# Kernel optimization log

Measured on AMD Instinct MI355X. Metric: run time of the kernel, lower is better.

The kernel has to match this reference:

```python
import jax, jax.numpy as jnp
import numpy as np

NUM_HEADS = 16


def setup_inputs() -> dict:
    key = jax.random.key(0)
    k1, k2, k3 = jax.random.split(key, 3)
    T, B, E = 2048, 2, 1024
    x = jax.random.normal(k1, (T, B, E), dtype=jnp.float32)
    in_proj_w = jax.random.normal(k2, (E, 3 * E), dtype=jnp.float32) * (E ** -0.5)
    in_proj_b = jnp.zeros((3 * E,), dtype=jnp.float32)
    out_w = jax.random.normal(k3, (E, E), dtype=jnp.float32) * (E ** -0.5)
    out_b = jnp.zeros((E,), dtype=jnp.float32)
    return {"x": x, "in_proj_w": in_proj_w, "in_proj_b": in_proj_b,
            "out_w": out_w, "out_b": out_b}


def reference(x, in_proj_w, in_proj_b, out_w, out_b):
    # x: (tgt_len, bsz, embed_dim) -- seq-first, self-attention (q is k is v)
    T, B, E = x.shape
    H = NUM_HEADS
    D = E // H
    scaling = D ** -0.5
    # packed in-projection: einsum('bne,ef->bnf') over (T,B,E)
    proj = jnp.einsum('tbe,ef->tbf', x, in_proj_w) + in_proj_b
    q, k, v = jnp.split(proj, 3, axis=-1)  # each (T, B, E)
    # reshape to (T, B*H, D) then transpose to (B*H, T, D)
    q = q.reshape(T, B * H, D).transpose(1, 0, 2)
    k = k.reshape(T, B * H, D).transpose(1, 0, 2)
    v = v.reshape(T, B * H, D).transpose(1, 0, 2)
    # full O(T^2) attention matrix, scaling applied after QK^T as in source
    attn = jnp.einsum('bie,bje->bij', q, k) * scaling  # (B*H, T, T)
    attn = jax.nn.softmax(attn, axis=-1)
    out = jnp.einsum('bij,bje->bie', attn, v)  # (B*H, T, D)
    # faithful to source: reshape directly (no head transpose-back)
    out = out.reshape(B, T, E)
    out = jnp.einsum('bte,ef->btf', out, out_w) + out_b
    return out
```

## Files before the change

### kernel.cpp

```cpp
#include <hip/hip_runtime.h>
#include <stdint.h>

#define TSEQ 2048
#define NB 2
#define EMB 1024
#define NHEAD 16
#define HDIM 64
#define KSPLIT 4
#define NT (TSEQ / KSPLIT / 64)
#define QSCALE 0.18033688f

typedef __bf16 bf16x8 __attribute__((ext_vector_type(8)));
typedef __bf16 bf16x4 __attribute__((ext_vector_type(4)));
typedef float f32x4 __attribute__((ext_vector_type(4)));
typedef float f32x16 __attribute__((ext_vector_type(16)));
typedef unsigned int u32x4 __attribute__((ext_vector_type(4)));

__device__ __forceinline__ void gload_lds16(const void* g, void* lds) {
    __builtin_amdgcn_global_load_lds(
        (const __attribute__((address_space(1))) unsigned int*)g,
        (__attribute__((address_space(3))) unsigned int*)lds, 16, 0, 0);
}

__device__ __forceinline__ float fast_exp2(float x) {
#if __has_builtin(__builtin_amdgcn_exp2f)
    return __builtin_amdgcn_exp2f(x);
#else
    return exp2f(x);
#endif
}

__device__ __forceinline__ unsigned cvt_pk_bf16(float lo, float hi) {
    unsigned r;
    asm("v_cvt_pk_bf16_f32 %0, %1, %2" : "=v"(r) : "v"(lo), "v"(hi));
    return r;
}

__device__ __forceinline__ void swap32(unsigned& a, unsigned& b) {
    asm("v_permlane32_swap_b32 %0, %1" : "+v"(a), "+v"(b));
}

__device__ __forceinline__ bf16x8 as_bf16x8(u32x4 u) {
    union { u32x4 u; bf16x8 h; } c;
    c.u = u;
    return c.h;
}

__global__ __launch_bounds__(256) void prep_kernel(
    const float* __restrict__ x, const float* __restrict__ w_in,
    const float* __restrict__ w_out,
    __bf16* __restrict__ xb, __bf16* __restrict__ wiT, __bf16* __restrict__ whT)
{
    __shared__ float tile[32][33];
    int bid = blockIdx.x;
    const int tid = threadIdx.x;
    if (bid < 4096) {
        const size_t idx = ((size_t)bid * 256 + tid) * 4;
        float4 v = *(const float4*)(x + idx);
        bf16x4 o = { (__bf16)v.x, (__bf16)v.y, (__bf16)v.z, (__bf16)v.w };
        *(bf16x4*)(xb + idx) = o;
        return;
    }
    bid -= 4096;
    int bx = bid & 127;
    const int by = bid >> 7;
    const float* src; __bf16* dst; int sn;
    if (bx < 96) { src = w_in;  dst = wiT; sn = 3072; }
    else         { bx -= 96; src = w_out; dst = whT; sn = 1024; }
    const int tx = tid & 31, ty = tid >> 5;
    #pragma unroll
    for (int i = 0; i < 4; ++i)
        tile[ty + i * 8][tx] = src[(size_t)(by * 32 + ty + i * 8) * sn + bx * 32 + tx];
    __syncthreads();
    #pragma unroll
    for (int i = 0; i < 4; ++i) {
        float v = tile[tx][ty + i * 8];
        dst[(size_t)(bx * 32 + ty + i * 8) * 1024 + by * 32 + tx] = (__bf16)v;
    }
}

__global__ __launch_bounds__(256) void gemm_qkv_kernel(
    const __bf16* __restrict__ A, const __bf16* __restrict__ BT,
    const float* __restrict__ bias,
    __bf16* __restrict__ Oq, __bf16* __restrict__ Ok, __bf16* __restrict__ Ov)
{
    __shared__ __align__(16) __bf16 As[128 * 64];
    __shared__ __align__(16) __bf16 Bs[128 * 64];
    const int tid = threadIdx.x;
    const int wave = tid >> 6, lane = tid & 63;
    const int l16 = lane & 15, quad = lane >> 4;
    const int wm = wave >> 1, wn = wave & 1;
    const int m0 = blockIdx.y * 128, n0 = blockIdx.x * 128;

    f32x4 acc[4][4];
    #pragma unroll
    for (int mt = 0; mt < 4; ++mt)
        #pragma unroll
        for (int nt = 0; nt < 4; ++nt)
            #pragma unroll
            for (int r = 0; r < 4; ++r) acc[mt][nt][r] = 0.f;

    int smrow[4], schunk[4], sbase[4];
    #pragma unroll
    for (int i = 0; i < 4; ++i) {
        int linear = (wave * 4 + i) * 64 + lane;
        smrow[i] = linear >> 3;
        schunk[i] = (linear & 7) ^ (smrow[i] & 7);
        sbase[i] = (wave * 4 + i) * 512;
    }

    for (int k0 = 0; k0 < 1024; k0 += 64) {
        #pragma unroll
        for (int i = 0; i < 4; ++i) {
            gload_lds16(A + (size_t)(m0 + smrow[i]) * 1024 + k0 + schunk[i] * 8,
                        As + sbase[i]);
            gload_lds16(BT + (size_t)(n0 + smrow[i]) * 1024 + k0 + schunk[i] * 8,
                        Bs + sbase[i]);
        }
        __syncthreads();
        #pragma unroll
        for (int kk = 0; kk < 2; ++kk) {
            bf16x8 am[4], bn[4];
            #pragma unroll
            for (int mt = 0; mt < 4; ++mt) {
                int row = wm * 64 + mt * 16 + l16;
                int c = (kk * 4 + quad) ^ (row & 7);
                am[mt] = *(const bf16x8*)(As + row * 64 + c * 8);
            }
            #pragma unroll
            for (int nt = 0; nt < 4; ++nt) {
                int row = wn * 64 + nt * 16 + l16;
                int c = (kk * 4 + quad) ^ (row & 7);
                bn[nt] = *(const bf16x8*)(Bs + row * 64 + c * 8);
            }
            #pragma unroll
            for (int mt = 0; mt < 4; ++mt)
                #pragma unroll
                for (int nt = 0; nt < 4; ++nt)
                    acc[mt][nt] = __builtin_amdgcn_mfma_f32_16x16x32_bf16(
                        am[mt], bn[nt], acc[mt][nt], 0, 0, 0);
        }
        __syncthreads();
    }

    #pragma unroll
    for (int nt = 0; nt < 4; ++nt) {
        const int col = n0 + wn * 64 + nt * 16 + l16;
        const float bv = bias[col];
        const int sec = col >> 10, f = col & 1023;
        const int h = f >> 6, d = f & 63;
        #pragma unroll
        for (int mt = 0; mt < 4; ++mt)
            #pragma unroll
            for (int r = 0; r < 4; ++r) {
                const int row = m0 + wm * 64 + mt * 16 + quad * 4 + r;
                float v = acc[mt][nt][r] + bv;
                const int t = row >> 1, b = row & 1;
                const int bh = b * NHEAD + h;
                const size_t idx = ((size_t)bh * TSEQ + t) * HDIM + d;
                if (sec == 0)
                    Oq[idx] = (__bf16)(v * QSCALE);
                else if (sec == 1)
                    Ok[idx] = (__bf16)v;
                else
                    Ov[idx] = (__bf16)v;
            }
    }
}

__global__ __launch_bounds__(256) void vtrans_kernel(
    const __bf16* __restrict__ V, __bf16* __restrict__ Vt)
{
    __shared__ __bf16 T[64 * 67];
    const int bh = blockIdx.y;
    const int t0 = blockIdx.x * 64;
    const int tid = threadIdx.x;
    const int r = tid >> 2;
    const int c = (tid & 3) * 16;
    const __bf16* src = V + ((size_t)bh * TSEQ + t0 + r) * HDIM + c;
    bf16x8 a = *(const bf16x8*)src;
    bf16x8 b = *(const bf16x8*)(src + 8);
    #pragma unroll
    for (int j = 0; j < 8; ++j) {
        T[r * 67 + c + j] = a[j];
        T[r * 67 + c + 8 + j] = b[j];
    }
    __syncthreads();
    const int dr = tid >> 2;
    const int tc = (tid & 3) * 16;
    bf16x8 o0, o1;
    #pragma unroll
    for (int j = 0; j < 8; ++j) {
        o0[j] = T[(tc + j) * 67 + dr];
        o1[j] = T[(tc + 8 + j) * 67 + dr];
    }
    __bf16* dst = Vt + ((size_t)bh * HDIM + dr) * TSEQ + t0 + tc;
    *(bf16x8*)dst = o0;
    *(bf16x8*)(dst + 8) = o1;
}

__global__ __launch_bounds__(256, 2) void attn_mfma_kernel(
    const __bf16* __restrict__ Q, const __bf16* __restrict__ K,
    const __bf16* __restrict__ Vt,
    __bf16* __restrict__ O0, __bf16* __restrict__ O1,
    __bf16* __restrict__ O2, __bf16* __restrict__ O3,
    float* __restrict__ L0, float* __restrict__ L1,
    float* __restrict__ L2, float* __restrict__ L3)
{
    __shared__ __align__(16) __bf16 Ks[2][64 * 64];
    __shared__ __align__(16) __bf16 Vs[2][64 * 64];

    const int tid  = threadIdx.x;
    const int wave = tid >> 6;
    const int lane = tid & 63;
    const int l31  = lane & 31;
    const int hi   = lane >> 5;
    const int m7   = l31 & 7;

    const int lid = blockIdx.x;
    const int xcd = lid & 7;
    const int j   = lid >> 3;
    const int grp = xcd * 16 + (j >> 3);
    const int qb  = j & 7;
    const int bh  = grp >> 2;
    const int z   = grp & 3;

    const int q0   = qb * 256 + wave * 64;
    const int kbase0 = z * (TSEQ / KSPLIT);

    __bf16* __restrict__ Opart = (z == 0) ? O0 : (z == 1) ? O1 : (z == 2) ? O2 : O3;
    float*  __restrict__ Lpart = (z == 0) ? L0 : (z == 1) ? L1 : (z == 2) ? L2 : L3;

    bf16x8 qf[2][4];
    #pragma unroll
    for (int g = 0; g < 2; ++g) {
        const __bf16* Qrow =
            Q + ((size_t)bh * TSEQ + q0 + g * 32 + l31) * HDIM + 8 * hi;
        #pragma unroll
        for (int c = 0; c < 4; ++c)
            qf[g][c] = *(const bf16x8*)(Qrow + 16 * c);
    }

    f32x16 Oacc[2][2];
    #pragma unroll
    for (int g = 0; g < 2; ++g)
        #pragma unroll
        for (int dt = 0; dt < 2; ++dt)
            #pragma unroll
            for (int r = 0; r < 16; ++r) Oacc[g][dt][r] = 0.f;
    float l4[2][4] = {{0.f, 0.f, 0.f, 0.f}, {0.f, 0.f, 0.f, 0.f}};

    const __bf16* Kbase = K + ((size_t)bh * TSEQ + kbase0) * HDIM;
    const __bf16* Vbase = Vt + (size_t)bh * HDIM * TSEQ + kbase0;

    int srow[2], schk[2];
    #pragma unroll
    for (int i = 0; i < 2; ++i) {
        const int s = wave * 2 + i;
        srow[i] = s * 8 + (lane >> 3);
        schk[i] = (lane & 7) ^ (srow[i] & 7);
    }

#define STAGE(buf, kt)                                                        \
    {                                                                         \
        _Pragma("unroll")                                                     \
        for (int i = 0; i < 2; ++i) {                                         \
            const int s = wave * 2 + i;                                       \
            gload_lds16(Kbase + (size_t)((kt) * 64 + srow[i]) * HDIM          \
                            + schk[i] * 8,                                    \
                        &Ks[buf][s * 512]);                                   \
            gload_lds16(Vbase + (size_t)srow[i] * TSEQ + (kt) * 64            \
                            + schk[i] * 8,                                    \
                        &Vs[buf][s * 512]);                                   \
        }                                                                     \
    }

#define SOFTMAX(sa, g, s)                                                     \
    {                                                                         \
        float p[16];                                                          \
        _Pragma("unroll")                                                     \
        for (int r = 0; r < 16; ++r) {                                        \
            p[r] = fast_exp2((sa)[r]);                                        \
            l4[g][r & 3] += p[r];                                             \
        }                                                                     \
        unsigned x[8];                                                        \
        _Pragma("unroll")                                                     \
        for (int i = 0; i < 8; ++i)                                           \
            x[i] = cvt_pk_bf16(p[2 * i], p[2 * i + 1]);                       \
        swap32(x[0], x[2]); swap32(x[1], x[3]);                               \
        swap32(x[4], x[6]); swap32(x[5], x[7]);                               \
        pa[g][2 * (s)][0] = x[0]; pa[g][2 * (s)][1] = x[1];                   \
        pa[g][2 * (s)][2] = x[2]; pa[g][2 * (s)][3] = x[3];                   \
        pa[g][2 * (s) + 1][0] = x[4]; pa[g][2 * (s) + 1][1] = x[5];           \
        pa[g][2 * (s) + 1][2] = x[6]; pa[g][2 * (s) + 1][3] = x[7];           \
    }

    STAGE(0, 0);

    for (int kt = 0; kt < NT; ++kt) {
        const int b = kt & 1;
        __syncthreads();
        if (kt + 1 < NT) STAGE(b ^ 1, kt + 1);

        u32x4 pa[2][4];
        #pragma unroll
        for (int s = 0; s < 2; ++s) {
            f32x16 sa0, sa1;
            #pragma unroll
            for (int r = 0; r < 16; ++r) { sa0[r] = 0.f; sa1[r] = 0.f; }
            #pragma unroll
            for (int c = 0; c < 4; ++c) {
                bf16x8 kf = *(const bf16x8*)(
                    &Ks[b][(32 * s + l31) * 64 + (((c << 1) | hi) ^ m7) * 8]);
                sa0 = __builtin_amdgcn_mfma_f32_32x32x16_bf16(
                    kf, qf[0][c], sa0, 0, 0, 0);
                sa1 = __builtin_amdgcn_mfma_f32_32x32x16_bf16(
                    kf, qf[1][c], sa1, 0, 0, 0);
            }
            SOFTMAX(sa0, 0, s);
            SOFTMAX(sa1, 1, s);
        }

        #pragma unroll
        for (int dt = 0; dt < 2; ++dt)
            #pragma unroll
            for (int ks = 0; ks < 4; ++ks) {
                bf16x8 vf = *(const bf16x8*)(
                    &Vs[b][(dt * 32 + l31) * 64 + (((ks << 1) | hi) ^ m7) * 8]);
                Oacc[0][dt] = __builtin_amdgcn_mfma_f32_32x32x16_bf16(
                    as_bf16x8(pa[0][ks]), vf, Oacc[0][dt], 0, 0, 0);
                Oacc[1][dt] = __builtin_amdgcn_mfma_f32_32x32x16_bf16(
                    as_bf16x8(pa[1][ks]), vf, Oacc[1][dt], 0, 0, 0);
            }
    }
#undef STAGE
#undef SOFTMAX

    #pragma unroll
    for (int g = 0; g < 2; ++g) {
        float v = (l4[g][0] + l4[g][1]) + (l4[g][2] + l4[g][3]);
        v += __shfl_xor(v, 32);
        if (hi == 0)
            Lpart[(size_t)bh * TSEQ + q0 + g * 32 + l31] = v;
    }

    const size_t base = ((size_t)bh * TSEQ + q0) * HDIM;
    #pragma unroll
    for (int g = 0; g < 2; ++g)
        #pragma unroll
        for (int dt = 0; dt < 2; ++dt)
            #pragma unroll
            for (int r = 0; r < 16; ++r) {
                const int q = g * 32 + (r & 3) + 8 * (r >> 2) + 4 * hi;
                Opart[base + (size_t)q * HDIM + dt * 32 + l31] =
                    (__bf16)Oacc[g][dt][r];
            }
}

__global__ __launch_bounds__(256) void normalize_kernel(
    const __bf16* __restrict__ O0, const __bf16* __restrict__ O1,
    const __bf16* __restrict__ O2, const __bf16* __restrict__ O3,
    const float* __restrict__ L0, const float* __restrict__ L1,
    const float* __restrict__ L2, const float* __restrict__ L3,
    __bf16* __restrict__ Ob)
{
    const size_t gid = (size_t)blockIdx.x * 256 + threadIdx.x;
    const size_t idx = gid * 8;
    const size_t qi = idx >> 6;
    const float inv = 1.f / (L0[qi] + L1[qi] + L2[qi] + L3[qi]);
    bf16x8 a = *(const bf16x8*)(O0 + idx);
    bf16x8 b = *(const bf16x8*)(O1 + idx);
    bf16x8 c = *(const bf16x8*)(O2 + idx);
    bf16x8 d = *(const bf16x8*)(O3 + idx);
    bf16x8 o;
    #pragma unroll
    for (int j = 0; j < 8; ++j)
        o[j] = (__bf16)((((float)a[j] + (float)b[j]) +
                         ((float)c[j] + (float)d[j])) * inv);
    *(bf16x8*)(Ob + idx) = o;
}

__global__ __launch_bounds__(256) void gemm_out_kernel(
    const __bf16* __restrict__ A, const __bf16* __restrict__ BT,
    const float* __restrict__ bias, float* __restrict__ out)
{
    __shared__ __align__(16) __bf16 As[128 * 64];
    __shared__ __align__(16) __bf16 Bs[128 * 64];
    const int tid = threadIdx.x;
    const int wave = tid >> 6, lane = tid & 63;
    const int l16 = lane & 15, quad = lane >> 4;
    const int wm = wave >> 1, wn = wave & 1;
    const int m0 = blockIdx.y * 128, n0 = blockIdx.x * 128;

    f32x4 acc[4][4];
    #pragma unroll
    for (int mt = 0; mt < 4; ++mt)
        #pragma unroll
        for (int nt = 0; nt < 4; ++nt)
            #pragma unroll
            for (int r = 0; r < 4; ++r) acc[mt][nt][r] = 0.f;

    int smrow[4], schunk[4], sbase[4];
    #pragma unroll
    for (int i = 0; i < 4; ++i) {
        int linear = (wave * 4 + i) * 64 + lane;
        smrow[i] = linear >> 3;
        schunk[i] = (linear & 7) ^ (smrow[i] & 7);
        sbase[i] = (wave * 4 + i) * 512;
    }

    for (int k0 = 0; k0 < 1024; k0 += 64) {
        #pragma unroll
        for (int i = 0; i < 4; ++i) {
            gload_lds16(A + (size_t)(m0 + smrow[i]) * 1024 + k0 + schunk[i] * 8,
                        As + sbase[i]);
            gload_lds16(BT + (size_t)(n0 + smrow[i]) * 1024 + k0 + schunk[i] * 8,
                        Bs + sbase[i]);
        }
        __syncthreads();
        #pragma unroll
        for (int kk = 0; kk < 2; ++kk) {
            bf16x8 am[4], bn[4];
            #pragma unroll
            for (int mt = 0; mt < 4; ++mt) {
                int row = wm * 64 + mt * 16 + l16;
                int c = (kk * 4 + quad) ^ (row & 7);
                am[mt] = *(const bf16x8*)(As + row * 64 + c * 8);
            }
            #pragma unroll
            for (int nt = 0; nt < 4; ++nt) {
                int row = wn * 64 + nt * 16 + l16;
                int c = (kk * 4 + quad) ^ (row & 7);
                bn[nt] = *(const bf16x8*)(Bs + row * 64 + c * 8);
            }
            #pragma unroll
            for (int mt = 0; mt < 4; ++mt)
                #pragma unroll
                for (int nt = 0; nt < 4; ++nt)
                    acc[mt][nt] = __builtin_amdgcn_mfma_f32_16x16x32_bf16(
                        am[mt], bn[nt], acc[mt][nt], 0, 0, 0);
        }
        __syncthreads();
    }

    #pragma unroll
    for (int nt = 0; nt < 4; ++nt) {
        const int col = n0 + wn * 64 + nt * 16 + l16;
        const float bv = bias[col];
        #pragma unroll
        for (int mt = 0; mt < 4; ++mt)
            #pragma unroll
            for (int r = 0; r < 4; ++r) {
                const int row = m0 + wm * 64 + mt * 16 + quad * 4 + r;
                out[(size_t)row * 1024 + col] = acc[mt][nt][r] + bv;
            }
    }
}

extern "C" void kernel_launch(void* const* d_in, const int* in_sizes, int n_in,
                              void* d_out, int out_size, void* d_ws, size_t ws_size,
                              hipStream_t stream) {
    const float* x     = (const float*)d_in[0];
    const float* w_in  = (const float*)d_in[1];
    const float* b_in  = (const float*)d_in[2];
    const float* w_out = (const float*)d_in[3];
    const float* b_out = (const float*)d_in[4];
    float* out = (float*)d_out;

    const size_t M1 = (size_t)1024 * 1024;
    __bf16* ws  = (__bf16*)d_ws;
    __bf16* xb  = ws;
    __bf16* wiT = xb  + 4 * M1;
    __bf16* whT = wiT + 3 * M1;
    __bf16* Qb  = whT + 1 * M1;
    __bf16* Kb  = Qb  + 4 * M1;
    __bf16* Vt  = Kb  + 4 * M1;
    __bf16* O0  = Vt  + 4 * M1;
    __bf16* O1  = O0  + 4 * M1;
    float*  L0  = (float*)(O1 + 4 * M1);
    float*  L1  = L0 + 65536;
    float*  L2  = L1 + 65536;
    float*  L3  = L2 + 65536;
    __bf16* Vb  = (__bf16*)d_out;
    __bf16* O2  = (__bf16*)d_out;
    __bf16* O3  = O2 + 4 * M1;
    __bf16* Ob  = xb;

    prep_kernel<<<8192, 256, 0, stream>>>(x, w_in, w_out, xb, wiT, whT);
    gemm_qkv_kernel<<<dim3(24, 32), 256, 0, stream>>>(
        xb, wiT, b_in, Qb, Kb, Vb);
    vtrans_kernel<<<dim3(32, 32), 256, 0, stream>>>(Vb, Vt);
    attn_mfma_kernel<<<dim3(1024), 256, 0, stream>>>(
        Qb, Kb, Vt, O0, O1, O2, O3, L0, L1, L2, L3);
    normalize_kernel<<<2048, 256, 0, stream>>>(
        O0, O1, O2, O3, L0, L1, L2, L3, Ob);
    gemm_out_kernel<<<dim3(8, 32), 256, 0, stream>>>(
        Ob, whT, b_out, out);
}
```

Baseline: 200.9 us.

## Use 512-thread attention blocks with triple-buffered K/V staging and MFMA priority

The attention kernel now runs 8 waves per block covering 512 query rows, so each staged K/V tile is shared by twice as many waves and each wave issues one load per tile. K/V staging moves from double to triple buffering with a two-tile prefetch distance, using an explicit vmcnt wait plus s_barrier in place of __syncthreads. s_setprio is raised around the MFMA sections so they are favoured over softmax work from other waves. In exchange LDS per block grows, the launch bound asks for 4 blocks of 512 threads per CU, which tightens the register budget, and the hand-written waitcnt depends on the exact number of outstanding loads.

Result: slower. 427.5 us (+112.8%).

```diff
diff --git a/kernel.cpp b/kernel.cpp
--- a/kernel.cpp
+++ b/kernel.cpp
@@ -199,7 +199,7 @@
     *(bf16x8*)(dst + 8) = o1;
 }
 
-__global__ __launch_bounds__(256, 2) void attn_mfma_kernel(
+__global__ __launch_bounds__(512, 4) void attn_mfma_kernel(
     const __bf16* __restrict__ Q, const __bf16* __restrict__ K,
     const __bf16* __restrict__ Vt,
     __bf16* __restrict__ O0, __bf16* __restrict__ O1,
@@ -207,8 +207,8 @@
     float* __restrict__ L0, float* __restrict__ L1,
     float* __restrict__ L2, float* __restrict__ L3)
 {
-    __shared__ __align__(16) __bf16 Ks[2][64 * 64];
-    __shared__ __align__(16) __bf16 Vs[2][64 * 64];
+    __shared__ __align__(16) __bf16 Ks[3][64 * 64];
+    __shared__ __align__(16) __bf16 Vs[3][64 * 64];
 
     const int tid  = threadIdx.x;
     const int wave = tid >> 6;
@@ -220,12 +220,12 @@
     const int lid = blockIdx.x;
     const int xcd = lid & 7;
     const int j   = lid >> 3;
-    const int grp = xcd * 16 + (j >> 3);
-    const int qb  = j & 7;
+    const int grp = xcd * 16 + (j >> 2);
+    const int qb  = j & 3;
     const int bh  = grp >> 2;
     const int z   = grp & 3;
 
-    const int q0   = qb * 256 + wave * 64;
+    const int q0   = qb * 512 + wave * 64;
     const int kbase0 = z * (TSEQ / KSPLIT);
 
     __bf16* __restrict__ Opart = (z == 0) ? O0 : (z == 1) ? O1 : (z == 2) ? O2 : O3;
@@ -253,26 +253,15 @@
     const __bf16* Kbase = K + ((size_t)bh * TSEQ + kbase0) * HDIM;
     const __bf16* Vbase = Vt + (size_t)bh * HDIM * TSEQ + kbase0;
 
-    int srow[2], schk[2];
-    #pragma unroll
-    for (int i = 0; i < 2; ++i) {
-        const int s = wave * 2 + i;
-        srow[i] = s * 8 + (lane >> 3);
-        schk[i] = (lane & 7) ^ (srow[i] & 7);
-    }
+    const int srow = wave * 8 + (lane >> 3);
+    const int schk = (lane & 7) ^ (srow & 7);
 
 #define STAGE(buf, kt)                                                        \
     {                                                                         \
-        _Pragma("unroll")                                                     \
-        for (int i = 0; i < 2; ++i) {                                         \
-            const int s = wave * 2 + i;                                       \
-            gload_lds16(Kbase + (size_t)((kt) * 64 + srow[i]) * HDIM          \
-                            + schk[i] * 8,                                    \
-                        &Ks[buf][s * 512]);                                   \
-            gload_lds16(Vbase + (size_t)srow[i] * TSEQ + (kt) * 64            \
-                            + schk[i] * 8,                                    \
-                        &Vs[buf][s * 512]);                                   \
-        }                                                                     \
+        gload_lds16(Kbase + (size_t)((kt) * 64 + srow) * HDIM + schk * 8,     \
+                    &Ks[buf][wave * 512]);                                    \
+        gload_lds16(Vbase + (size_t)srow * TSEQ + (kt) * 64 + schk * 8,       \
+                    &Vs[buf][wave * 512]);                                    \
     }
 
 #define SOFTMAX(sa, g, s)                                                     \
@@ -296,11 +285,18 @@
     }
 
     STAGE(0, 0);
+    STAGE(1, 1);
+
+    int rb = 0;
+    int sb = 2;
 
     for (int kt = 0; kt < NT; ++kt) {
-        const int b = kt & 1;
-        __syncthreads();
-        if (kt + 1 < NT) STAGE(b ^ 1, kt + 1);
+        if (kt + 1 < NT)
+            asm volatile("s_waitcnt vmcnt(2)\n\ts_barrier" ::: "memory");
+        else
+            asm volatile("s_waitcnt vmcnt(0)\n\ts_barrier" ::: "memory");
+
+        if (kt + 2 < NT) STAGE(sb, kt + 2);
 
         u32x4 pa[2][4];
         #pragma unroll
@@ -308,30 +304,37 @@
             f32x16 sa0, sa1;
             #pragma unroll
             for (int r = 0; r < 16; ++r) { sa0[r] = 0.f; sa1[r] = 0.f; }
+            __builtin_amdgcn_s_setprio(1);
             #pragma unroll
             for (int c = 0; c < 4; ++c) {
                 bf16x8 kf = *(const bf16x8*)(
-                    &Ks[b][(32 * s + l31) * 64 + (((c << 1) | hi) ^ m7) * 8]);
+                    &Ks[rb][(32 * s + l31) * 64 + (((c << 1) | hi) ^ m7) * 8]);
                 sa0 = __builtin_amdgcn_mfma_f32_32x32x16_bf16(
                     kf, qf[0][c], sa0, 0, 0, 0);
                 sa1 = __builtin_amdgcn_mfma_f32_32x32x16_bf16(
                     kf, qf[1][c], sa1, 0, 0, 0);
             }
+            __builtin_amdgcn_s_setprio(0);
             SOFTMAX(sa0, 0, s);
             SOFTMAX(sa1, 1, s);
         }
 
+        __builtin_amdgcn_s_setprio(1);
         #pragma unroll
         for (int dt = 0; dt < 2; ++dt)
             #pragma unroll
             for (int ks = 0; ks < 4; ++ks) {
                 bf16x8 vf = *(const bf16x8*)(
-                    &Vs[b][(dt * 32 + l31) * 64 + (((ks << 1) | hi) ^ m7) * 8]);
+                    &Vs[rb][(dt * 32 + l31) * 64 + (((ks << 1) | hi) ^ m7) * 8]);
                 Oacc[0][dt] = __builtin_amdgcn_mfma_f32_32x32x16_bf16(
                     as_bf16x8(pa[0][ks]), vf, Oacc[0][dt], 0, 0, 0);
                 Oacc[1][dt] = __builtin_amdgcn_mfma_f32_32x32x16_bf16(
                     as_bf16x8(pa[1][ks]), vf, Oacc[1][dt], 0, 0, 0);
             }
+        __builtin_amdgcn_s_setprio(0);
+
+        rb = (rb == 2) ? 0 : rb + 1;
+        sb = (sb == 2) ? 0 : sb + 1;
     }
 #undef STAGE
 #undef SOFTMAX
@@ -490,7 +493,7 @@
     gemm_qkv_kernel<<<dim3(24, 32), 256, 0, stream>>>(
         xb, wiT, b_in, Qb, Kb, Vb);
     vtrans_kernel<<<dim3(32, 32), 256, 0, stream>>>(Vb, Vt);
-    attn_mfma_kernel<<<dim3(1024), 256, 0, stream>>>(
+    attn_mfma_kernel<<<dim3(512), 512, 0, stream>>>(
         Qb, Kb, Vt, O0, O1, O2, O3, L0, L1, L2, L3);
     normalize_kernel<<<2048, 256, 0, stream>>>(
         O0, O1, O2, O3, L0, L1, L2, L3, Ob);
```
